# Kernel optimization log

Hardware: AMD Instinct MI355X
Metric: run time of the kernel (lower is better)

## Reference

```python
import jax, jax.numpy as jnp
import numpy as np

N = 1024      # number of nodes
D = 128       # d_x
H = 8         # num_heads


def setup_inputs() -> dict:
    key = jax.random.key(0)
    ks = jax.random.split(key, 7)
    s = (D * H) ** -0.5
    return {
        "x": jax.random.normal(ks[0], (N, D), dtype=jnp.float32),
        "spatial_encoding": jax.random.normal(ks[1], (N, N), dtype=jnp.float32),
        "edge_encoding": jax.random.normal(ks[2], (N, N), dtype=jnp.float32),
        "Wq": jax.random.normal(ks[3], (D * H, D), dtype=jnp.float32) * s,
        "Wk": jax.random.normal(ks[4], (D * H, D), dtype=jnp.float32) * s,
        "Wv": jax.random.normal(ks[5], (D * H, D), dtype=jnp.float32) * s,
        "Wo": jax.random.normal(ks[6], (D, D * H), dtype=jnp.float32) * s,
    }


def reference(x, spatial_encoding, edge_encoding, Wq, Wk, Wv, Wo):
    n, d = x.shape
    h = Wq.shape[0] // d
    scale = d ** -0.5
    # Linear (no bias), then the module's peculiar view: [n, d*h] -> [d, n, h]
    q = (x @ Wq.T).reshape(d, n, h)            # [d, n, h]
    k = (x @ Wk.T).reshape(d, n, h)            # [d, n, h]
    v = (x @ Wv.T).reshape(d, n, h)            # [d, n, h]
    # a = q @ k^T over head dim: [d, n, n]
    a = jnp.einsum('dnh,dmh->dnm', q, k) * scale
    a = a + spatial_encoding + edge_encoding   # [n,n] biases broadcast over d
    a = jax.nn.softmax(a, axis=2)
    # dropout is identity at inference
    out = jnp.einsum('dnm,dmh->dnh', a, v)     # [d, n, h]
    out = out.reshape(n, h * d)                # row-major reshape, same as torch
    return out @ Wo.T                          # [n, d]
```

## Files before the change

### kernel.cpp

```cpp
#include <hip/hip_runtime.h>
#include <hip/hip_bf16.h>
#include <math.h>

#define N_NODES 1024
#define D_DIM   128
#define H_HEADS 8
#define DH      1024

typedef short  short8 __attribute__((ext_vector_type(8)));
typedef float  f32x16 __attribute__((ext_vector_type(16)));
typedef float  f32x4  __attribute__((ext_vector_type(4)));

static __device__ __forceinline__ unsigned short f2bf(float x) {
    __hip_bfloat16 h = __float2bfloat16(x);
    return *reinterpret_cast<unsigned short*>(&h);
}
static __device__ __forceinline__ unsigned cvt_pk_bf16(float lo, float hi) {
    unsigned r;
    asm("v_cvt_pk_bf16_f32 %0, %1, %2" : "=v"(r) : "v"(lo), "v"(hi));
    return r;
}
static __device__ __forceinline__ void permlane32_swap(unsigned &a, unsigned &b) {
    asm("v_permlane32_swap_b32 %0, %1" : "+v"(a), "+v"(b));
}
static __device__ __forceinline__ float fast_exp2(float x) {
    float r;
    asm("v_exp_f32 %0, %1" : "=v"(r) : "v"(x));
    return r;
}

__global__ __launch_bounds__(256, 1) void prep_kernel(
        const float* __restrict__ x,  const float* __restrict__ Wq,
        const float* __restrict__ Wk, const float* __restrict__ Wv,
        const float* __restrict__ sp, const float* __restrict__ ed,
        const float* __restrict__ Wo,
        unsigned short* __restrict__ Qb, unsigned short* __restrict__ Kb,
        unsigned short* __restrict__ Vb, unsigned short* __restrict__ Bq16,
        unsigned short* __restrict__ Woh, unsigned short* __restrict__ Wol) {
    __shared__ float tile[32][33];
    const int u   = blockIdx.x;
    const int tid = threadIdx.x;

    if (u < 768) {
        const int lane = tid & 63, wvi = tid >> 6;
        const int l31 = lane & 31, hi = lane >> 5;
        const int m   = u >> 8;
        const int rem = u & 255;
        const int rb0 = (rem & 7) * 128 + wvi * 32;
        const int col = (rem >> 3) * 32 + l31;
        const float* W        = (m == 0) ? Wq : (m == 1) ? Wk : Wv;
        unsigned short* Out   = (m == 0) ? Qb : (m == 1) ? Kb : Vb;
        const float osc = (m == 0) ? 0.12751879523173864f : 1.0f;

        const float* xrow = x + (size_t)(rb0 + l31) * 128 + 8 * hi;
        const float* wrow = W + (size_t)col * 128 + 8 * hi;

        f32x16 acc = {};
        #pragma unroll
        for (int ks = 0; ks < 8; ++ks) {
            float4 xa = *reinterpret_cast<const float4*>(xrow + ks * 16);
            float4 xb = *reinterpret_cast<const float4*>(xrow + ks * 16 + 4);
            float4 wa = *reinterpret_cast<const float4*>(wrow + ks * 16);
            float4 wb = *reinterpret_cast<const float4*>(wrow + ks * 16 + 4);
            union { short8 s8; unsigned uu[4]; } af, bf;
            af.uu[0] = cvt_pk_bf16(xa.x, xa.y); af.uu[1] = cvt_pk_bf16(xa.z, xa.w);
            af.uu[2] = cvt_pk_bf16(xb.x, xb.y); af.uu[3] = cvt_pk_bf16(xb.z, xb.w);
            bf.uu[0] = cvt_pk_bf16(wa.x, wa.y); bf.uu[1] = cvt_pk_bf16(wa.z, wa.w);
            bf.uu[2] = cvt_pk_bf16(wb.x, wb.y); bf.uu[3] = cvt_pk_bf16(wb.z, wb.w);
            acc = __builtin_amdgcn_mfma_f32_32x32x16_bf16(af.s8, bf.s8, acc, 0, 0, 0);
        }
        #pragma unroll
        for (int i = 0; i < 16; ++i) {
            int mm = (i & 3) + 8 * (i >> 2) + 4 * hi;
            Out[(size_t)(rb0 + mm) * DH + col] = f2bf(acc[i] * osc);
        }
    } else if (u < 1792) {
        const int b2 = u - 768;
        const int cb = b2 & 31, rb = b2 >> 5;
        const float L2E = 1.4426950408889634f;
        for (int i = tid; i < 1024; i += 256) {
            int rr = i >> 5, cc = i & 31;
            size_t g = (size_t)(rb * 32 + rr) * 1024 + cb * 32 + cc;
            tile[rr][cc] = (sp[g] + ed[g]) * L2E;
        }
        __syncthreads();
        const int rr  = tid >> 3, rem = tid & 7;
        const int hi  = rem >> 2, g = rem & 3;
        const int c0  = 8 * g + 4 * hi;
        uint2 v;
        v.x = cvt_pk_bf16(tile[rr][c0],     tile[rr][c0 + 1]);
        v.y = cvt_pk_bf16(tile[rr][c0 + 2], tile[rr][c0 + 3]);
        reinterpret_cast<uint2*>(Bq16)[((size_t)(cb * 2 + hi) * 1024 + rb * 32 + rr) * 4 + g] = v;
    } else {
        const int b2 = u - 1792;
        const size_t base = (size_t)b2 * 4096 + (size_t)tid * 16;
        #pragma unroll
        for (int t = 0; t < 4; ++t) {
            float4 w = *reinterpret_cast<const float4*>(Wo + base + t * 4);
            float ww[4] = { w.x, w.y, w.z, w.w };
            unsigned short h4[4], l4[4];
            #pragma unroll
            for (int j = 0; j < 4; ++j) {
                unsigned uv = __float_as_uint(ww[j]);
                h4[j] = (unsigned short)(uv >> 16);
                l4[j] = f2bf(ww[j] - __uint_as_float(uv & 0xFFFF0000u));
            }
            *reinterpret_cast<uint2*>(Woh + base + t * 4) = *reinterpret_cast<uint2*>(h4);
            *reinterpret_cast<uint2*>(Wol + base + t * 4) = *reinterpret_cast<uint2*>(l4);
        }
    }
}

static __device__ __forceinline__ void stage_vt(const unsigned short* __restrict__ src,
                                                char* base, int tid) {
    #pragma unroll
    for (int it = 0; it < 2; ++it) {
        int pr = it * 256 + tid;
        short8 v0 = *reinterpret_cast<const short8*>(src + (size_t)(2 * pr) * 8);
        short8 v1 = *reinterpret_cast<const short8*>(src + (size_t)(2 * pr + 1) * 8);
        #pragma unroll
        for (int h = 0; h < 8; ++h) {
            unsigned d = (unsigned)(unsigned short)v0[h] |
                         ((unsigned)(unsigned short)v1[h] << 16);
            *reinterpret_cast<unsigned*>(base + h * 2048 + ((4 * pr) ^ (h << 4))) = d;
        }
    }
    reinterpret_cast<unsigned*>(base + 16384)[tid]       = 0x3F803F80u;
    reinterpret_cast<unsigned*>(base + 16384)[tid + 256] = 0x3F803F80u;
}

static __device__ __forceinline__ f32x16 load_bias16(const uint4* b) {
    uint4 ua = b[0], ub = b[1];
    unsigned uu[8] = { ua.x, ua.y, ua.z, ua.w, ub.x, ub.y, ub.z, ub.w };
    f32x16 o;
    #pragma unroll
    for (int i = 0; i < 8; ++i) {
        o[2 * i]     = __uint_as_float(uu[i] << 16);
        o[2 * i + 1] = __uint_as_float(uu[i] & 0xFFFF0000u);
    }
    return o;
}

static __device__ __forceinline__ void pack_p(const float* p, short8& pb1, short8& pb2) {
    unsigned u0 = cvt_pk_bf16(p[0],  p[1]);
    unsigned u1 = cvt_pk_bf16(p[2],  p[3]);
    unsigned u2 = cvt_pk_bf16(p[4],  p[5]);
    unsigned u3 = cvt_pk_bf16(p[6],  p[7]);
    unsigned u4 = cvt_pk_bf16(p[8],  p[9]);
    unsigned u5 = cvt_pk_bf16(p[10], p[11]);
    unsigned u6 = cvt_pk_bf16(p[12], p[13]);
    unsigned u7 = cvt_pk_bf16(p[14], p[15]);
    permlane32_swap(u0, u2);
    permlane32_swap(u1, u3);
    permlane32_swap(u4, u6);
    permlane32_swap(u5, u7);
    union { short8 s8; unsigned uu[4]; } a, b;
    a.uu[0] = u0; a.uu[1] = u1; a.uu[2] = u2; a.uu[3] = u3;
    b.uu[0] = u4; b.uu[1] = u5; b.uu[2] = u6; b.uu[3] = u7;
    pb1 = a.s8; pb2 = b.s8;
}

static __device__ __forceinline__ void attn_epilogue(const f32x16& oa, int dd, int r, int hi,
                                                     unsigned short* __restrict__ Oh) {
    const float rl = 1.f / oa[4];
    unsigned short h4[4];
    #pragma unroll
    for (int i = 0; i < 4; ++i) h4[i] = f2bf(oa[i] * rl);
    size_t off = (size_t)dd * 8192 + (size_t)r * 8 + 4 * hi;
    *reinterpret_cast<uint2*>(Oh + off) = *reinterpret_cast<uint2*>(h4);
}

__global__ __launch_bounds__(256, 1) void attn2_kernel(
        const unsigned short* __restrict__ Qb, const unsigned short* __restrict__ Kb,
        const unsigned short* __restrict__ Vb, const unsigned short* __restrict__ Bq16,
        unsigned short* __restrict__ Oh) {
    __shared__ __align__(16) char smraw[36864];
    const int un = blockIdx.x, tid = threadIdx.x;
    const int rbx = un & 7, dp = un >> 3;
    const int lane = tid & 63, wvi = tid >> 6;
    const int l31 = lane & 31, hi = lane >> 5;

    stage_vt(Vb + (size_t)(2 * dp) * 8192,     smraw,         tid);
    stage_vt(Vb + (size_t)(2 * dp + 1) * 8192, smraw + 18432, tid);
    __syncthreads();

    const int r = rbx * 128 + wvi * 32 + l31;
    short8 qf0 = {}, qf1 = {};
    if (!hi) {
        qf0 = *reinterpret_cast<const short8*>(Qb + (size_t)(2 * dp)     * 8192 + (size_t)r * 8);
        qf1 = *reinterpret_cast<const short8*>(Qb + (size_t)(2 * dp + 1) * 8192 + (size_t)r * 8);
    }
    f32x16 o0 = {}, o1 = {};
    const unsigned short* kp0 = Kb + (size_t)(2 * dp) * 8192 + (size_t)l31 * 8;
    const unsigned short* kp1 = kp0 + 8192;
    const uint4* bp = reinterpret_cast<const uint4*>(Bq16) + ((size_t)hi * 1024 + r) * 2;
    const int vrow = (l31 < 8) ? l31 : 8;
    const char* vb0 = smraw + vrow * 2048;
    const char* vb1 = smraw + 18432 + vrow * 2048;
    const int vswz = vrow << 4;

    auto step2 = [&](int cbv, const f32x16& bias, const short8& k0, const short8& k1) {
        f32x16 s0 = __builtin_amdgcn_mfma_f32_32x32x16_bf16(k0, qf0, bias, 0, 0, 0);
        f32x16 s1 = __builtin_amdgcn_mfma_f32_32x32x16_bf16(k1, qf1, bias, 0, 0, 0);
        short8 va1 = *reinterpret_cast<const short8*>(vb0 + ((cbv * 64 + 16 * hi)      ^ vswz));
        short8 va2 = *reinterpret_cast<const short8*>(vb0 + ((cbv * 64 + 32 + 16 * hi) ^ vswz));
        short8 vc1 = *reinterpret_cast<const short8*>(vb1 + ((cbv * 64 + 16 * hi)      ^ vswz));
        short8 vc2 = *reinterpret_cast<const short8*>(vb1 + ((cbv * 64 + 32 + 16 * hi) ^ vswz));
        float p0[16], p1[16];
        #pragma unroll
        for (int i = 0; i < 16; ++i) { p0[i] = fast_exp2(s0[i]); p1[i] = fast_exp2(s1[i]); }
        short8 pa1, pa2, pb1, pb2;
        pack_p(p0, pa1, pa2);
        pack_p(p1, pb1, pb2);
        o0 = __builtin_amdgcn_mfma_f32_32x32x16_bf16(va1, pa1, o0, 0, 0, 0);
        o1 = __builtin_amdgcn_mfma_f32_32x32x16_bf16(vc1, pb1, o1, 0, 0, 0);
        o0 = __builtin_amdgcn_mfma_f32_32x32x16_bf16(va2, pa2, o0, 0, 0, 0);
        o1 = __builtin_amdgcn_mfma_f32_32x32x16_bf16(vc2, pb2, o1, 0, 0, 0);
    };

    f32x16 bA = load_bias16(bp), bB = load_bias16(bp + 4096);
    short8 kA0 = *reinterpret_cast<const short8*>(kp0);
    short8 kA1 = *reinterpret_cast<const short8*>(kp1);
    short8 kB0 = *reinterpret_cast<const short8*>(kp0 + 256);
    short8 kB1 = *reinterpret_cast<const short8*>(kp1 + 256);
    for (int cb = 0; cb < 32; cb += 2) {
        step2(cb, bA, kA0, kA1);
        if (cb < 30) {
            bA  = load_bias16(bp + (size_t)(cb + 2) * 4096);
            kA0 = *reinterpret_cast<const short8*>(kp0 + (size_t)(cb + 2) * 256);
            kA1 = *reinterpret_cast<const short8*>(kp1 + (size_t)(cb + 2) * 256);
        }
        step2(cb + 1, bB, kB0, kB1);
        if (cb < 30) {
            bB  = load_bias16(bp + (size_t)(cb + 3) * 4096);
            kB0 = *reinterpret_cast<const short8*>(kp0 + (size_t)(cb + 3) * 256);
            kB1 = *reinterpret_cast<const short8*>(kp1 + (size_t)(cb + 3) * 256);
        }
    }
    attn_epilogue(o0, 2 * dp,     r, hi, Oh);
    attn_epilogue(o1, 2 * dp + 1, r, hi, Oh);
}

__global__ __launch_bounds__(256) void oproj_kernel(
        const unsigned short* __restrict__ Oh,
        const unsigned short* __restrict__ Woh, const unsigned short* __restrict__ Wol,
        float* __restrict__ out) {
    __shared__ float red[4][256];
    const int u = blockIdx.x, tid = threadIdx.x;
    const int lane = tid & 63, wvi = tid >> 6;
    const int l15 = lane & 15, kg = lane >> 4;
    const int rbase = (u & 63) * 16, cbase = (u >> 6) * 16;

    const unsigned short* ah_p = Oh  + (size_t)(rbase + l15) * 1024 + wvi * 256 + kg * 8;
    const unsigned short* bh_p = Woh + (size_t)(cbase + l15) * 1024 + wvi * 256 + kg * 8;
    const unsigned short* bl_p = Wol + (size_t)(cbase + l15) * 1024 + wvi * 256 + kg * 8;

    f32x4 acc = {};
    #pragma unroll
    for (int ks = 0; ks < 8; ++ks) {
        short8 ah = *reinterpret_cast<const short8*>(ah_p + ks * 32);
        short8 bh = *reinterpret_cast<const short8*>(bh_p + ks * 32);
        short8 bl = *reinterpret_cast<const short8*>(bl_p + ks * 32);
        acc = __builtin_amdgcn_mfma_f32_16x16x32_bf16(ah, bh, acc, 0, 0, 0);
        acc = __builtin_amdgcn_mfma_f32_16x16x32_bf16(ah, bl, acc, 0, 0, 0);
    }
    #pragma unroll
    for (int i = 0; i < 4; ++i)
        red[wvi][(kg * 4 + i) * 16 + l15] = acc[i];
    __syncthreads();
    float v = red[0][tid & 255] + red[1][tid & 255] + red[2][tid & 255] + red[3][tid & 255];
    out[(size_t)(rbase + (tid >> 4)) * D_DIM + cbase + (tid & 15)] = v;
}

extern "C" void kernel_launch(void* const* d_in, const int* in_sizes, int n_in,
                              void* d_out, int out_size, void* d_ws, size_t ws_size,
                              hipStream_t stream) {
    const float* x  = (const float*)d_in[0];
    const float* sp = (const float*)d_in[1];
    const float* ed = (const float*)d_in[2];
    const float* Wq = (const float*)d_in[3];
    const float* Wk = (const float*)d_in[4];
    const float* Wv = (const float*)d_in[5];
    const float* Wo = (const float*)d_in[6];
    float* out = (float*)d_out;

    float* ws = (float*)d_ws;
    const size_t M = (size_t)N_NODES * DH;
    unsigned short* Bq16 = (unsigned short*)ws;
    unsigned short* Qb = Bq16 + M;
    unsigned short* Kb = Qb + M;
    unsigned short* Vb = Kb + M;
    unsigned short* Oh = Vb + M;
    unsigned short* Woh = Oh + M;
    unsigned short* Wol = Woh + 131072;

    prep_kernel<<<dim3(1824), 256, 0, stream>>>(x, Wq, Wk, Wv, sp, ed, Wo,
                                                Qb, Kb, Vb, Bq16, Woh, Wol);
    attn2_kernel<<<dim3(512), 256, 0, stream>>>(Qb, Kb, Vb, Bq16, Oh);
    oproj_kernel<<<dim3(512), 256, 0, stream>>>(Oh, Woh, Wol, out);
}
```

Baseline: 61.89 us.

## Split attention key dimension across two blocks and combine partials in new kernel

The attention kernel now splits the 1024 keys into two halves, each processed by a separate block (grid 8x64x2), and writes unnormalized fp32 partial outputs and row sums to workspace. A new combine kernel sums the two partials, normalizes, and converts to bf16 for the output projection. This doubles the block count (1024 vs 512) to fill more CUs and halves the LDS per block. In exchange it adds an extra launch and extra global traffic for the fp32 partials. The softmax stays valid only because no running max is used.

Result: slower. 64.76 us (+4.6%).

```diff
diff --git a/kernel.cpp b/kernel.cpp
--- a/kernel.cpp
+++ b/kernel.cpp
@@ -111,22 +111,18 @@
     }
 }
 
-static __device__ __forceinline__ void stage_vt(const unsigned short* __restrict__ src,
-                                                char* base, int tid) {
-    #pragma unroll
-    for (int it = 0; it < 2; ++it) {
-        int pr = it * 256 + tid;
-        short8 v0 = *reinterpret_cast<const short8*>(src + (size_t)(2 * pr) * 8);
-        short8 v1 = *reinterpret_cast<const short8*>(src + (size_t)(2 * pr + 1) * 8);
-        #pragma unroll
-        for (int h = 0; h < 8; ++h) {
-            unsigned d = (unsigned)(unsigned short)v0[h] |
-                         ((unsigned)(unsigned short)v1[h] << 16);
-            *reinterpret_cast<unsigned*>(base + h * 2048 + ((4 * pr) ^ (h << 4))) = d;
-        }
-    }
-    reinterpret_cast<unsigned*>(base + 16384)[tid]       = 0x3F803F80u;
-    reinterpret_cast<unsigned*>(base + 16384)[tid + 256] = 0x3F803F80u;
+static __device__ __forceinline__ void stage_vt_half(const unsigned short* __restrict__ src,
+                                                     char* base, int tid) {
+    int pr = tid;
+    short8 v0 = *reinterpret_cast<const short8*>(src + (size_t)(2 * pr) * 8);
+    short8 v1 = *reinterpret_cast<const short8*>(src + (size_t)(2 * pr + 1) * 8);
+    #pragma unroll
+    for (int h = 0; h < 8; ++h) {
+        unsigned d = (unsigned)(unsigned short)v0[h] |
+                     ((unsigned)(unsigned short)v1[h] << 16);
+        *reinterpret_cast<unsigned*>(base + h * 1024 + ((4 * pr) ^ (h << 4))) = d;
+    }
+    reinterpret_cast<unsigned*>(base + 8 * 1024)[tid] = 0x3F803F80u;
 }
 
 static __device__ __forceinline__ f32x16 load_bias16(const uint4* b) {
@@ -160,28 +156,18 @@
     pb1 = a.s8; pb2 = b.s8;
 }
 
-static __device__ __forceinline__ void attn_epilogue(const f32x16& oa, int dd, int r, int hi,
-                                                     unsigned short* __restrict__ Oh) {
-    const float rl = 1.f / oa[4];
-    unsigned short h4[4];
-    #pragma unroll
-    for (int i = 0; i < 4; ++i) h4[i] = f2bf(oa[i] * rl);
-    size_t off = (size_t)dd * 8192 + (size_t)r * 8 + 4 * hi;
-    *reinterpret_cast<uint2*>(Oh + off) = *reinterpret_cast<uint2*>(h4);
-}
-
 __global__ __launch_bounds__(256, 1) void attn2_kernel(
         const unsigned short* __restrict__ Qb, const unsigned short* __restrict__ Kb,
         const unsigned short* __restrict__ Vb, const unsigned short* __restrict__ Bq16,
-        unsigned short* __restrict__ Oh) {
-    __shared__ __align__(16) char smraw[36864];
-    const int un = blockIdx.x, tid = threadIdx.x;
-    const int rbx = un & 7, dp = un >> 3;
+        float* __restrict__ Opart, float* __restrict__ Lpart) {
+    __shared__ __align__(16) char smraw[18432];
+    const int tid = threadIdx.x;
+    const int rbx = blockIdx.x, dp = blockIdx.y, ch = blockIdx.z;
     const int lane = tid & 63, wvi = tid >> 6;
     const int l31 = lane & 31, hi = lane >> 5;
 
-    stage_vt(Vb + (size_t)(2 * dp) * 8192,     smraw,         tid);
-    stage_vt(Vb + (size_t)(2 * dp + 1) * 8192, smraw + 18432, tid);
+    stage_vt_half(Vb + (size_t)(2 * dp) * 8192     + (size_t)ch * 4096, smraw,        tid);
+    stage_vt_half(Vb + (size_t)(2 * dp + 1) * 8192 + (size_t)ch * 4096, smraw + 9216, tid);
     __syncthreads();
 
     const int r = rbx * 128 + wvi * 32 + l31;
@@ -191,12 +177,13 @@
         qf1 = *reinterpret_cast<const short8*>(Qb + (size_t)(2 * dp + 1) * 8192 + (size_t)r * 8);
     }
     f32x16 o0 = {}, o1 = {};
-    const unsigned short* kp0 = Kb + (size_t)(2 * dp) * 8192 + (size_t)l31 * 8;
+    const unsigned short* kp0 = Kb + (size_t)(2 * dp) * 8192 + (size_t)(ch * 512 + l31) * 8;
     const unsigned short* kp1 = kp0 + 8192;
-    const uint4* bp = reinterpret_cast<const uint4*>(Bq16) + ((size_t)hi * 1024 + r) * 2;
+    const uint4* bp = reinterpret_cast<const uint4*>(Bq16)
+                      + ((size_t)(ch * 32 + hi) * 1024 + r) * 2;
     const int vrow = (l31 < 8) ? l31 : 8;
-    const char* vb0 = smraw + vrow * 2048;
-    const char* vb1 = smraw + 18432 + vrow * 2048;
+    const char* vb0 = smraw + vrow * 1024;
+    const char* vb1 = smraw + 9216 + vrow * 1024;
     const int vswz = vrow << 4;
 
     auto step2 = [&](int cbv, const f32x16& bias, const short8& k0, const short8& k1) {
@@ -223,22 +210,49 @@
     short8 kA1 = *reinterpret_cast<const short8*>(kp1);
     short8 kB0 = *reinterpret_cast<const short8*>(kp0 + 256);
     short8 kB1 = *reinterpret_cast<const short8*>(kp1 + 256);
-    for (int cb = 0; cb < 32; cb += 2) {
+    for (int cb = 0; cb < 16; cb += 2) {
         step2(cb, bA, kA0, kA1);
-        if (cb < 30) {
+        if (cb < 14) {
             bA  = load_bias16(bp + (size_t)(cb + 2) * 4096);
             kA0 = *reinterpret_cast<const short8*>(kp0 + (size_t)(cb + 2) * 256);
             kA1 = *reinterpret_cast<const short8*>(kp1 + (size_t)(cb + 2) * 256);
         }
         step2(cb + 1, bB, kB0, kB1);
-        if (cb < 30) {
+        if (cb < 14) {
             bB  = load_bias16(bp + (size_t)(cb + 3) * 4096);
             kB0 = *reinterpret_cast<const short8*>(kp0 + (size_t)(cb + 3) * 256);
             kB1 = *reinterpret_cast<const short8*>(kp1 + (size_t)(cb + 3) * 256);
         }
     }
-    attn_epilogue(o0, 2 * dp,     r, hi, Oh);
-    attn_epilogue(o1, 2 * dp + 1, r, hi, Oh);
+
+    #pragma unroll
+    for (int s = 0; s < 2; ++s) {
+        const f32x16& oa = s ? o1 : o0;
+        const int dd = 2 * dp + s;
+        size_t off = (size_t)ch * 1048576 + (size_t)dd * 8192 + (size_t)r * 8 + 4 * hi;
+        *reinterpret_cast<float4*>(Opart + off) = make_float4(oa[0], oa[1], oa[2], oa[3]);
+        if (!hi) Lpart[(size_t)ch * 131072 + (size_t)dd * 1024 + r] = oa[4];
+    }
+}
+
+__global__ __launch_bounds__(256) void combine_kernel(const float* __restrict__ Opart,
+                                                      const float* __restrict__ Lpart,
+                                                      unsigned short* __restrict__ Oh) {
+    const int gid = blockIdx.x * 256 + threadIdx.x;
+    const float4* p1 = reinterpret_cast<const float4*>(Opart) + (size_t)gid * 2;
+    const float4* p2 = reinterpret_cast<const float4*>(Opart + 1048576) + (size_t)gid * 2;
+    float4 a0 = p1[0], a1 = p1[1], b0 = p2[0], b1 = p2[1];
+    const float rl = 1.f / (Lpart[gid] + Lpart[131072 + gid]);
+    union { short8 s8; unsigned short us[8]; } h8;
+    h8.us[0] = f2bf((a0.x + b0.x) * rl);
+    h8.us[1] = f2bf((a0.y + b0.y) * rl);
+    h8.us[2] = f2bf((a0.z + b0.z) * rl);
+    h8.us[3] = f2bf((a0.w + b0.w) * rl);
+    h8.us[4] = f2bf((a1.x + b1.x) * rl);
+    h8.us[5] = f2bf((a1.y + b1.y) * rl);
+    h8.us[6] = f2bf((a1.z + b1.z) * rl);
+    h8.us[7] = f2bf((a1.w + b1.w) * rl);
+    *reinterpret_cast<short8*>(Oh + (size_t)gid * 8) = h8.s8;
 }
 
 __global__ __launch_bounds__(256) void oproj_kernel(
@@ -293,9 +307,12 @@
     unsigned short* Oh = Vb + M;
     unsigned short* Woh = Oh + M;
     unsigned short* Wol = Woh + 131072;
+    float* Opart = (float*)(Wol + 131072);
+    float* Lpart = Opart + 2 * M;
 
     prep_kernel<<<dim3(1824), 256, 0, stream>>>(x, Wq, Wk, Wv, sp, ed, Wo,
                                                 Qb, Kb, Vb, Bq16, Woh, Wol);
-    attn2_kernel<<<dim3(512), 256, 0, stream>>>(Qb, Kb, Vb, Bq16, Oh);
+    attn2_kernel<<<dim3(8, 64, 2), 256, 0, stream>>>(Qb, Kb, Vb, Bq16, Opart, Lpart);
+    combine_kernel<<<dim3(512), 256, 0, stream>>>(Opart, Lpart, Oh);
     oproj_kernel<<<dim3(512), 256, 0, stream>>>(Oh, Woh, Wol, out);
 }
```
